# Kernel optimization log

Hardware: AMD Instinct MI355X
Metric: run time of the kernel (lower is better)

## Reference

```python
import jax, jax.numpy as jnp
import numpy as np

N, IN_F, OUT_F = 8192, 512, 256
NEG_INF = -9e15
LEAKY_SLOPE = 0.25


def setup_inputs() -> dict:
    key = jax.random.key(0)
    k1, k2, k3, k4, k5, k6 = jax.random.split(key, 6)
    inp = {
        "input": jax.random.normal(k1, (N, IN_F), dtype=jnp.float32),
        "adj": jax.random.randint(k2, (N, N), 0, 2, dtype=jnp.int32),
        # learned params (xavier-normal-ish scale)
        "weights": jax.random.normal(k3, (IN_F, OUT_F), dtype=jnp.float32) * (2.0 / (IN_F + OUT_F)) ** 0.5,
        "a1": jax.random.normal(k4, (OUT_F, 1), dtype=jnp.float32) * (2.0 / (OUT_F + 1)) ** 0.5,
        "a2": jax.random.normal(k5, (OUT_F, 1), dtype=jnp.float32) * (2.0 / (OUT_F + 1)) ** 0.5,
        "bias": jax.random.uniform(k6, (OUT_F,), dtype=jnp.float32, minval=-1.0 / OUT_F ** 0.5, maxval=1.0 / OUT_F ** 0.5),
    }
    return inp


def reference(input, adj, weights, a1, a2, bias):
    # h = input @ W  : [N, out]
    h = input @ weights
    # e[i,j] = leaky_relu((h@a1)[i] + (h@a2)[j])  : [N, N] via broadcast
    e1 = h @ a1  # [N,1]
    e2 = h @ a2  # [N,1]
    e = e1 + e2.T
    e = jnp.where(e > 0, e, LEAKY_SLOPE * e)
    # mask non-edges, row softmax (dropout omitted: deterministic reference)
    scores = jnp.where(adj > 0, e, NEG_INF)
    attention = jax.nn.softmax(scores, axis=1)
    # aggregate + bias
    return attention @ h + bias
```

## Files before the change

### kernel.cpp

```cpp
#include <hip/hip_runtime.h>
#include <hip/hip_fp16.h>

typedef __attribute__((ext_vector_type(8))) short short8;
typedef __attribute__((ext_vector_type(4))) float floatx4;
typedef __attribute__((ext_vector_type(4))) unsigned int uintx4;
typedef __attribute__((ext_vector_type(2))) unsigned int uintx2;
typedef __attribute__((ext_vector_type(4))) int intx4;
typedef __attribute__((ext_vector_type(4))) unsigned short ushortx4;
typedef unsigned int u32;

#define NN 8192
#define KIN 512
#define COUT 256
#define SHIFT 16.0f

#define AS1 __attribute__((address_space(1)))
#define AS3 __attribute__((address_space(3)))

__device__ __forceinline__ void stage16(const void* g, void* l) {
  __builtin_amdgcn_global_load_lds((const AS1 u32*)g, (AS3 u32*)l, 16, 0, 0);
}

__device__ __forceinline__ unsigned int f2bf(float f) {
  unsigned int u = __float_as_uint(f);
  return (u + 0x7FFFu + ((u >> 16) & 1u)) >> 16;
}

__device__ __forceinline__ u32 pkbf(float lo, float hi) {
  u32 a = __float_as_uint(lo) + 0x8000u;
  u32 b = __float_as_uint(hi) + 0x8000u;
  return __builtin_amdgcn_perm(b, a, 0x07060302u);
}

__device__ __forceinline__ short8 pack8(const float* p) {
  uintx4 w;
  w.x = pkbf(p[0], p[1]);
  w.y = pkbf(p[2], p[3]);
  w.z = pkbf(p[4], p[5]);
  w.w = pkbf(p[6], p[7]);
  union { uintx4 u; short8 s; } cv; cv.u = w;
  return cv.s;
}

__global__ void k_cast_input(const float* __restrict__ in, ushortx4* __restrict__ out) {
  int idx = blockIdx.x * 256 + threadIdx.x;
  floatx4 v = ((const floatx4*)in)[idx];
  ushortx4 o;
  o.x = (unsigned short)f2bf(v.x);
  o.y = (unsigned short)f2bf(v.y);
  o.z = (unsigned short)f2bf(v.z);
  o.w = (unsigned short)f2bf(v.w);
  out[idx] = o;
}

__global__ void k_prep_w(const float* __restrict__ w, unsigned short* __restrict__ wt) {
  int idx = blockIdx.x * 256 + threadIdx.x;
  int k = idx >> 8, c = idx & 255;
  wt[c * KIN + k] = (unsigned short)f2bf(w[idx]);
}

__global__ __launch_bounds__(256)
void k_gemm_h(const unsigned short* __restrict__ inA, const unsigned short* __restrict__ wt,
              const float* __restrict__ a1, const float* __restrict__ a2,
              unsigned short* __restrict__ ht, float* __restrict__ e1, float* __restrict__ e2,
              float* __restrict__ A1, float* __restrict__ A2, u32* __restrict__ e2pk) {
  int wave = threadIdx.x >> 6;
  int lane = threadIdx.x & 63;
  int n = lane & 15, q = lane >> 4;
  int row0 = blockIdx.x * 64 + wave * 16;
  int mrow = row0 + n;

  floatx4 acc[16];
#pragma unroll
  for (int t = 0; t < 16; ++t) acc[t] = (floatx4){0.f, 0.f, 0.f, 0.f};

  for (int kc = 0; kc < KIN / 32; ++kc) {
    int k0 = kc * 32 + q * 8;
    short8 a = *(const short8*)(inA + (size_t)mrow * KIN + k0);
#pragma unroll
    for (int nt = 0; nt < 16; ++nt) {
      short8 b = *(const short8*)(wt + (size_t)(nt * 16 + n) * KIN + k0);
      acc[nt] = __builtin_amdgcn_mfma_f32_16x16x32_bf16(a, b, acc[nt], 0, 0, 0);
    }
  }

  int i0 = row0 + q * 4;
#pragma unroll
  for (int nt = 0; nt < 16; ++nt) {
    int c = nt * 16 + n;
    uintx2 pk;
    pk.x = f2bf(acc[nt][0]) | (f2bf(acc[nt][1]) << 16);
    pk.y = f2bf(acc[nt][2]) | (f2bf(acc[nt][3]) << 16);
    *(uintx2*)(ht + (size_t)c * NN + i0) = pk;
  }

  float s1[4] = {0.f, 0.f, 0.f, 0.f}, s2[4] = {0.f, 0.f, 0.f, 0.f};
#pragma unroll
  for (int nt = 0; nt < 16; ++nt) {
    float w1 = a1[nt * 16 + n];
    float w2 = a2[nt * 16 + n];
#pragma unroll
    for (int r = 0; r < 4; ++r) {
      s1[r] += acc[nt][r] * w1;
      s2[r] += acc[nt][r] * w2;
    }
  }
#pragma unroll
  for (int m = 1; m < 16; m <<= 1) {
#pragma unroll
    for (int r = 0; r < 4; ++r) {
      s1[r] += __shfl_xor(s1[r], m);
      s2[r] += __shfl_xor(s2[r], m);
    }
  }
  if (n == 0) {
#pragma unroll
    for (int r = 0; r < 4; ++r) {
      float v1 = s1[r], v2 = s2[r];
      e1[i0 + r] = v1;
      e2[i0 + r] = v2;
      A1[i0 + r] = __expf(v1 - 8.0f);
      A2[i0 + r] = __expf(0.25f * v1 - 8.0f);
      u32 b1 = f2bf(__expf(v2 - 8.0f));
      u32 b2 = f2bf(__expf(0.25f * v2 - 8.0f));
      e2pk[i0 + r] = (b1 << 16) | b2;
    }
  }
}

__global__ __launch_bounds__(256, 2)
void k_attn_fused(const int* __restrict__ adj, const unsigned short* __restrict__ ht,
                  const float* __restrict__ A1, const float* __restrict__ A2,
                  const u32* __restrict__ e2pk,
                  __half2* __restrict__ oph, float* __restrict__ Dpart) {
  __shared__ __align__(16) char smem[69632];
  u32* e2s = (u32*)(smem + 65536);

  int b = blockIdx.x;
  int rg = b >> 3, js = b & 7;
  int wave = threadIdx.x >> 6, lane = threadIdx.x & 63;
  int n = lane & 15, q = lane >> 4;
  int rowblock = rg * 128;
  int rowbase = rowblock + wave * 32;
  int jbeg = js * 1024;

  ((uintx4*)e2s)[threadIdx.x] = *(const uintx4*)(e2pk + jbeg + threadIdx.x * 4);

  float A1v0 = A1[rowbase + n],      A2v0 = A2[rowbase + n];
  float A1v1 = A1[rowbase + 16 + n], A2v1 = A2[rowbase + 16 + n];

  floatx4 acc[2][16];
  floatx4 accd[2];
#pragma unroll
  for (int t = 0; t < 2; ++t) {
    accd[t] = (floatx4){0.f, 0.f, 0.f, 0.f};
#pragma unroll
    for (int nt = 0; nt < 16; ++nt) acc[t][nt] = (floatx4){0.f, 0.f, 0.f, 0.f};
  }

  union { uintx4 u; short8 s; } onesu;
  onesu.u = (uintx4){0x3F803F80u, 0x3F803F80u, 0x3F803F80u, 0x3F803F80u};
  short8 ones = onesu.s;

  auto stage = [&](int ch, int buf) {
    int j0g = jbeg + ch * 32;
    char* hbase = smem + buf * 32768;
#pragma unroll
    for (int i = 0; i < 4; ++i) {
      int seg = wave * 256 + i * 64 + lane;
      int c = seg >> 2;
      int j8 = (seg & 3) * 8;
      stage16(ht + (size_t)c * NN + j0g + j8, hbase + (size_t)(wave * 256 + i * 64) * 16);
    }
    char* abase = hbase + 16384 + wave * 4096;
    const int* aw = adj + (size_t)(rowblock + wave * 32) * NN + j0g;
#pragma unroll
    for (int i = 0; i < 4; ++i) {
      stage16(aw + (size_t)(i * 8 + (lane & 7)) * NN + (lane >> 3) * 4, abase + i * 1024);
    }
  };

  int rlo = n & 7, rhi = n >> 3;

  stage(0, 0);
  asm volatile("s_waitcnt lgkmcnt(0)" ::: "memory");
  asm volatile("s_barrier" ::: "memory");

  for (int ch = 0; ch < 32; ++ch) {
    int cur = ch & 1;
    if (ch < 31) {
      stage(ch + 1, cur ^ 1);
      asm volatile("s_waitcnt vmcnt(8)" ::: "memory");
    } else {
      asm volatile("s_waitcnt vmcnt(0)" ::: "memory");
    }

    const char* ab = smem + cur * 32768 + 16384 + wave * 4096;
    intx4 a0a = *(const intx4*)(ab + rhi * 1024 + q * 256 + rlo * 16);
    intx4 a0b = *(const intx4*)(ab + rhi * 1024 + q * 256 + 128 + rlo * 16);
    intx4 a1a = *(const intx4*)(ab + 2048 + rhi * 1024 + q * 256 + rlo * 16);
    intx4 a1b = *(const intx4*)(ab + 2048 + rhi * 1024 + q * 256 + 128 + rlo * 16);

    uintx4 ba = *(const uintx4*)(e2s + ch * 32 + q * 8);
    uintx4 bb = *(const uintx4*)(e2s + ch * 32 + q * 8 + 4);
    u32 bw[8] = {ba.x, ba.y, ba.z, ba.w, bb.x, bb.y, bb.z, bb.w};

    float p0[8], p1[8];
#pragma unroll
    for (int jj = 0; jj < 8; ++jj) {
      int av0 = (jj < 4) ? a0a[jj] : a0b[jj - 4];
      int av1 = (jj < 4) ? a1a[jj] : a1b[jj - 4];
      float B1 = __uint_as_float(bw[jj] & 0xffff0000u);
      float B2 = __uint_as_float(bw[jj] << 16);
      float m10 = A1v0 * B1, m20 = A2v0 * B2;
      float m11 = A1v1 * B1, m21 = A2v1 * B2;
      float pm0 = fmaxf(m10, m20);
      float pm1 = fmaxf(m11, m21);
      p0[jj] = (av0 != 0) ? pm0 : 0.f;
      p1[jj] = (av1 != 0) ? pm1 : 0.f;
    }
    short8 af0 = pack8(p0);
    short8 af1 = pack8(p1);

    asm volatile("s_barrier" ::: "memory");

    const short8* lb = (const short8*)(smem + (size_t)cur * 32768);
#pragma unroll
    for (int t = 0; t < 16; ++t) {
      short8 bf = lb[t * 64 + n * 4 + q];
      acc[0][t] = __builtin_amdgcn_mfma_f32_16x16x32_bf16(af0, bf, acc[0][t], 0, 0, 0);
      acc[1][t] = __builtin_amdgcn_mfma_f32_16x16x32_bf16(af1, bf, acc[1][t], 0, 0, 0);
    }
    accd[0] = __builtin_amdgcn_mfma_f32_16x16x32_bf16(af0, ones, accd[0], 0, 0, 0);
    accd[1] = __builtin_amdgcn_mfma_f32_16x16x32_bf16(af1, ones, accd[1], 0, 0, 0);

    asm volatile("s_waitcnt lgkmcnt(0)" ::: "memory");
    asm volatile("s_barrier" ::: "memory");
  }

  if (n == 0) {
#pragma unroll
    for (int t2 = 0; t2 < 2; ++t2)
#pragma unroll
      for (int r = 0; r < 4; ++r)
        Dpart[(size_t)js * NN + rowbase + t2 * 16 + q * 4 + r] = accd[t2][r];
  }

#pragma unroll
  for (int t2 = 0; t2 < 2; ++t2) {
    int ibase = rowbase + t2 * 16 + q * 4;
#pragma unroll
    for (int nt = 0; nt < 16; ++nt) {
      int c = nt * 16 + n;
      oph[((size_t)js * 4096 + (ibase >> 1)) * 256 + c] =
          __floats2half2_rn(acc[t2][nt][0], acc[t2][nt][1]);
      oph[((size_t)js * 4096 + (ibase >> 1) + 1) * 256 + c] =
          __floats2half2_rn(acc[t2][nt][2], acc[t2][nt][3]);
    }
  }
}

__global__ void k_final_part(float* __restrict__ out, const __half2* __restrict__ oph,
                             const float* __restrict__ Dpart, const float* __restrict__ bias) {
  int i = blockIdx.x;
  int c = threadIdx.x;
  int hi = i & 1;
  float s = 0.f, d = 0.f;
#pragma unroll
  for (int js = 0; js < 8; ++js) {
    __half2 h2 = oph[((size_t)js * 4096 + (i >> 1)) * 256 + c];
    s += hi ? __high2float(h2) : __low2float(h2);
    d += Dpart[(size_t)js * NN + i];
  }
  out[(size_t)i * COUT + c] = s / fmaxf(d, 1e-37f) + bias[c];
}

__global__ __launch_bounds__(256, 2)
void k_attn_atomic(const int* __restrict__ adj, const unsigned short* __restrict__ ht,
                   const float* __restrict__ e1, const float* __restrict__ e2,
                   float* __restrict__ out_num, float* __restrict__ Dbuf) {
  int b = blockIdx.x;
  int rg = b >> 3, js = b & 7;
  int wave = threadIdx.x >> 6, lane = threadIdx.x & 63;
  int n = lane & 15, q = lane >> 4;
  int rowbase = rg * 128 + wave * 32;

  float e1v0 = e1[rowbase + n];
  float e1v1 = e1[rowbase + 16 + n];

  floatx4 acc[2][16];
#pragma unroll
  for (int t = 0; t < 2; ++t)
#pragma unroll
    for (int nt = 0; nt < 16; ++nt) acc[t][nt] = (floatx4){0.f, 0.f, 0.f, 0.f};

  float d0 = 0.f, d1 = 0.f;
  int jbeg = js * 1024;

  for (int ch = 0; ch < 32; ++ch) {
    int j0 = jbeg + ch * 32 + q * 8;
    floatx4 ea = *(const floatx4*)(e2 + j0);
    floatx4 eb = *(const floatx4*)(e2 + j0 + 4);
    float ev[8] = {ea.x, ea.y, ea.z, ea.w, eb.x, eb.y, eb.z, eb.w};

    intx4 A00 = *(const intx4*)(adj + (size_t)(rowbase + n) * NN + j0);
    intx4 A01 = *(const intx4*)(adj + (size_t)(rowbase + n) * NN + j0 + 4);
    intx4 A10 = *(const intx4*)(adj + (size_t)(rowbase + 16 + n) * NN + j0);
    intx4 A11 = *(const intx4*)(adj + (size_t)(rowbase + 16 + n) * NN + j0 + 4);

    float p0[8], p1[8];
#pragma unroll
    for (int jj = 0; jj < 8; ++jj) {
      int av0 = (jj < 4) ? A00[jj] : A01[jj - 4];
      int av1 = (jj < 4) ? A10[jj] : A11[jj - 4];
      float t0 = e1v0 + ev[jj];
      float t1 = e1v1 + ev[jj];
      float f0 = fmaxf(t0, 0.25f * t0);
      float f1 = fmaxf(t1, 0.25f * t1);
      float x0 = __expf(f0 - SHIFT);
      float x1 = __expf(f1 - SHIFT);
      p0[jj] = (av0 != 0) ? x0 : 0.f;
      p1[jj] = (av1 != 0) ? x1 : 0.f;
      d0 += p0[jj];
      d1 += p1[jj];
    }
    short8 af0 = pack8(p0);
    short8 af1 = pack8(p1);

#pragma unroll
    for (int g = 0; g < 2; ++g) {
      short8 bf[8];
#pragma unroll
      for (int t = 0; t < 8; ++t)
        bf[t] = *(const short8*)(ht + (size_t)((g * 8 + t) * 16 + n) * NN + j0);
#pragma unroll
      for (int t = 0; t < 8; ++t) {
        acc[0][g * 8 + t] = __builtin_amdgcn_mfma_f32_16x16x32_bf16(af0, bf[t], acc[0][g * 8 + t], 0, 0, 0);
        acc[1][g * 8 + t] = __builtin_amdgcn_mfma_f32_16x16x32_bf16(af1, bf[t], acc[1][g * 8 + t], 0, 0, 0);
      }
    }
  }

  d0 += __shfl_xor(d0, 16); d0 += __shfl_xor(d0, 32);
  d1 += __shfl_xor(d1, 16); d1 += __shfl_xor(d1, 32);
  if (lane < 16) {
    atomicAdd(Dbuf + rowbase + lane, d0);
    atomicAdd(Dbuf + rowbase + 16 + lane, d1);
  }

#pragma unroll
  for (int t2 = 0; t2 < 2; ++t2) {
#pragma unroll
    for (int nt = 0; nt < 16; ++nt) {
#pragma unroll
      for (int r = 0; r < 4; ++r) {
        int i = rowbase + t2 * 16 + q * 4 + r;
        atomicAdd(out_num + (size_t)i * COUT + nt * 16 + n, acc[t2][nt][r]);
      }
    }
  }
}

__global__ void k_final_atomic(float* __restrict__ out, const float* __restrict__ Dbuf,
                               const float* __restrict__ bias) {
  int idx = blockIdx.x * 256 + threadIdx.x;
  int i = idx >> 8, c = idx & 255;
  float d = fmaxf(Dbuf[i], 1e-37f);
  out[idx] = out[idx] / d + bias[c];
}

extern "C" void kernel_launch(void* const* d_in, const int* in_sizes, int n_in,
                              void* d_out, int out_size, void* d_ws, size_t ws_size,
                              hipStream_t stream) {
  const float* input   = (const float*)d_in[0];
  const int*   adj     = (const int*)d_in[1];
  const float* weights = (const float*)d_in[2];
  const float* a1      = (const float*)d_in[3];
  const float* a2      = (const float*)d_in[4];
  const float* bias    = (const float*)d_in[5];
  float* out = (float*)d_out;
  char* ws = (char*)d_ws;

  unsigned short* inA = (unsigned short*)(ws);
  unsigned short* wt  = (unsigned short*)(ws + 8388608);
  unsigned short* ht  = (unsigned short*)(ws + 8650752);
  float* e1    = (float*)(ws + 12845056);
  float* e2    = (float*)(ws + 12877824);
  float* A1    = (float*)(ws + 12910592);
  float* A2    = (float*)(ws + 12943360);
  u32*   e2pk  = (u32*)  (ws + 12976128);
  float* Dpart = (float*)(ws + 13008896);
  __half2* oph = (__half2*)(ws + 13271040);
  const size_t WS_NEEDED_PART = 13271040 + (size_t)8 * NN * COUT * 2;
  float* Dbuf = Dpart;

  k_cast_input<<<4096, 256, 0, stream>>>(input, (ushortx4*)inA);
  k_prep_w<<<512, 256, 0, stream>>>(weights, wt);
  k_gemm_h<<<128, 256, 0, stream>>>(inA, wt, a1, a2, ht, e1, e2, A1, A2, e2pk);

  if (ws_size >= WS_NEEDED_PART) {
    k_attn_fused<<<512, 256, 0, stream>>>(adj, ht, A1, A2, e2pk, oph, Dpart);
    k_final_part<<<8192, 256, 0, stream>>>(out, oph, Dpart, bias);
  } else {
    hipMemsetAsync(out, 0, (size_t)NN * COUT * sizeof(float), stream);
    hipMemsetAsync(Dbuf, 0, NN * sizeof(float), stream);
    k_attn_atomic<<<512, 256, 0, stream>>>(adj, ht, e1, e2, out, Dbuf);
    k_final_atomic<<<8192, 256, 0, stream>>>(out, Dbuf, bias);
  }
}
```

Measured before the change: 447.3 us.

## Pre-pack adjacency into a bitmask and merge the prep kernels

A combined prep kernel now does the input and weight bf16 casts and also packs the int32 adjacency matrix into one bit per edge. The attention kernel then loads a small per-block bitmask into LDS once, instead of staging int32 adjacency tiles every chunk. This frees LDS, reduces per-chunk global loads to the h tiles only, and moves the wait so it overlaps the probability computation. The cost is an extra streaming pass over adj, an extra bitmask buffer, and a larger workspace requirement; if the workspace is too small, the atomic fallback path runs instead.

Measured after the change: 466.7 us. 1.04x slower.

```diff
diff --git a/kernel.cpp b/kernel.cpp
--- a/kernel.cpp
+++ b/kernel.cpp
@@ -42,21 +42,38 @@
   return cv.s;
 }
 
-__global__ void k_cast_input(const float* __restrict__ in, ushortx4* __restrict__ out) {
-  int idx = blockIdx.x * 256 + threadIdx.x;
-  floatx4 v = ((const floatx4*)in)[idx];
-  ushortx4 o;
-  o.x = (unsigned short)f2bf(v.x);
-  o.y = (unsigned short)f2bf(v.y);
-  o.z = (unsigned short)f2bf(v.z);
-  o.w = (unsigned short)f2bf(v.w);
-  out[idx] = o;
-}
-
-__global__ void k_prep_w(const float* __restrict__ w, unsigned short* __restrict__ wt) {
-  int idx = blockIdx.x * 256 + threadIdx.x;
-  int k = idx >> 8, c = idx & 255;
-  wt[c * KIN + k] = (unsigned short)f2bf(w[idx]);
+__global__ __launch_bounds__(256)
+void k_prep(const float* __restrict__ in, ushortx4* __restrict__ inA4,
+            const float* __restrict__ w, unsigned short* __restrict__ wt,
+            const int* __restrict__ adj, u32* __restrict__ abit, int do_pack) {
+  int b = blockIdx.x;
+  if (b < 4096) {
+    int idx = b * 256 + threadIdx.x;
+    floatx4 v = ((const floatx4*)in)[idx];
+    ushortx4 o;
+    o.x = (unsigned short)f2bf(v.x);
+    o.y = (unsigned short)f2bf(v.y);
+    o.z = (unsigned short)f2bf(v.z);
+    o.w = (unsigned short)f2bf(v.w);
+    inA4[idx] = o;
+  } else if (b < 4608) {
+    int idx = (b - 4096) * 256 + threadIdx.x;
+    int k = idx >> 8, c = idx & 255;
+    wt[c * KIN + k] = (unsigned short)f2bf(w[idx]);
+  } else if (do_pack) {
+    int g = (b - 4608) * 256 + threadIdx.x;
+    const intx4* src = (const intx4*)adj + (size_t)g * 8;
+    u32 m = 0;
+#pragma unroll
+    for (int k = 0; k < 8; ++k) {
+      intx4 v = src[k];
+      m |= (u32)(v.x != 0) << (k * 4);
+      m |= (u32)(v.y != 0) << (k * 4 + 1);
+      m |= (u32)(v.z != 0) << (k * 4 + 2);
+      m |= (u32)(v.w != 0) << (k * 4 + 3);
+    }
+    abit[g] = m;
+  }
 }
 
 __global__ __launch_bounds__(256)
@@ -129,12 +146,13 @@
 }
 
 __global__ __launch_bounds__(256, 2)
-void k_attn_fused(const int* __restrict__ adj, const unsigned short* __restrict__ ht,
+void k_attn_fused(const u32* __restrict__ abit, const unsigned short* __restrict__ ht,
                   const float* __restrict__ A1, const float* __restrict__ A2,
                   const u32* __restrict__ e2pk,
                   __half2* __restrict__ oph, float* __restrict__ Dpart) {
-  __shared__ __align__(16) char smem[69632];
-  u32* e2s = (u32*)(smem + 65536);
+  __shared__ __align__(16) char smem[55296];
+  u32* e2s  = (u32*)(smem + 32768);
+  u32* bits = (u32*)(smem + 36864);
 
   int b = blockIdx.x;
   int rg = b >> 3, js = b & 7;
@@ -144,27 +162,9 @@
   int rowbase = rowblock + wave * 32;
   int jbeg = js * 1024;
 
-  ((uintx4*)e2s)[threadIdx.x] = *(const uintx4*)(e2pk + jbeg + threadIdx.x * 4);
-
-  float A1v0 = A1[rowbase + n],      A2v0 = A2[rowbase + n];
-  float A1v1 = A1[rowbase + 16 + n], A2v1 = A2[rowbase + 16 + n];
-
-  floatx4 acc[2][16];
-  floatx4 accd[2];
-#pragma unroll
-  for (int t = 0; t < 2; ++t) {
-    accd[t] = (floatx4){0.f, 0.f, 0.f, 0.f};
-#pragma unroll
-    for (int nt = 0; nt < 16; ++nt) acc[t][nt] = (floatx4){0.f, 0.f, 0.f, 0.f};
-  }
-
-  union { uintx4 u; short8 s; } onesu;
-  onesu.u = (uintx4){0x3F803F80u, 0x3F803F80u, 0x3F803F80u, 0x3F803F80u};
-  short8 ones = onesu.s;
-
   auto stage = [&](int ch, int buf) {
     int j0g = jbeg + ch * 32;
-    char* hbase = smem + buf * 32768;
+    char* hbase = smem + buf * 16384;
 #pragma unroll
     for (int i = 0; i < 4; ++i) {
       int seg = wave * 256 + i * 64 + lane;
@@ -172,34 +172,48 @@
       int j8 = (seg & 3) * 8;
       stage16(ht + (size_t)c * NN + j0g + j8, hbase + (size_t)(wave * 256 + i * 64) * 16);
     }
-    char* abase = hbase + 16384 + wave * 4096;
-    const int* aw = adj + (size_t)(rowblock + wave * 32) * NN + j0g;
-#pragma unroll
-    for (int i = 0; i < 4; ++i) {
-      stage16(aw + (size_t)(i * 8 + (lane & 7)) * NN + (lane >> 3) * 4, abase + i * 1024);
-    }
   };
 
-  int rlo = n & 7, rhi = n >> 3;
-
   stage(0, 0);
+
+  ((uintx4*)e2s)[threadIdx.x] = *(const uintx4*)(e2pk + jbeg + threadIdx.x * 4);
+
+  {
+    int r = threadIdx.x >> 1, half = threadIdx.x & 1;
+    const uintx4* src = (const uintx4*)(abit + (size_t)(rowblock + r) * 256 + js * 32 + half * 16);
+    uintx4* dst = (uintx4*)(bits + r * 36 + half * 16);
+#pragma unroll
+    for (int k2 = 0; k2 < 4; ++k2) dst[k2] = src[k2];
+  }
+
+  float A1v0 = A1[rowbase + n],      A2v0 = A2[rowbase + n];
+  float A1v1 = A1[rowbase + 16 + n], A2v1 = A2[rowbase + 16 + n];
+
+  floatx4 acc[2][16];
+  floatx4 accd[2];
+#pragma unroll
+  for (int t = 0; t < 2; ++t) {
+    accd[t] = (floatx4){0.f, 0.f, 0.f, 0.f};
+#pragma unroll
+    for (int nt = 0; nt < 16; ++nt) acc[t][nt] = (floatx4){0.f, 0.f, 0.f, 0.f};
+  }
+
+  union { uintx4 u; short8 s; } onesu;
+  onesu.u = (uintx4){0x3F803F80u, 0x3F803F80u, 0x3F803F80u, 0x3F803F80u};
+  short8 ones = onesu.s;
+
   asm volatile("s_waitcnt lgkmcnt(0)" ::: "memory");
   asm volatile("s_barrier" ::: "memory");
 
+  int row0i = (wave * 32 + n) * 36;
+  int row1i = (wave * 32 + 16 + n) * 36;
+
   for (int ch = 0; ch < 32; ++ch) {
     int cur = ch & 1;
-    if (ch < 31) {
-      stage(ch + 1, cur ^ 1);
-      asm volatile("s_waitcnt vmcnt(8)" ::: "memory");
-    } else {
-      asm volatile("s_waitcnt vmcnt(0)" ::: "memory");
-    }
-
-    const char* ab = smem + cur * 32768 + 16384 + wave * 4096;
-    intx4 a0a = *(const intx4*)(ab + rhi * 1024 + q * 256 + rlo * 16);
-    intx4 a0b = *(const intx4*)(ab + rhi * 1024 + q * 256 + 128 + rlo * 16);
-    intx4 a1a = *(const intx4*)(ab + 2048 + rhi * 1024 + q * 256 + rlo * 16);
-    intx4 a1b = *(const intx4*)(ab + 2048 + rhi * 1024 + q * 256 + 128 + rlo * 16);
+    if (ch < 31) stage(ch + 1, cur ^ 1);
+
+    u32 f0 = (bits[row0i + ch] >> (q * 8)) & 0xffu;
+    u32 f1 = (bits[row1i + ch] >> (q * 8)) & 0xffu;
 
     uintx4 ba = *(const uintx4*)(e2s + ch * 32 + q * 8);
     uintx4 bb = *(const uintx4*)(e2s + ch * 32 + q * 8 + 4);
@@ -208,23 +222,26 @@
     float p0[8], p1[8];
 #pragma unroll
     for (int jj = 0; jj < 8; ++jj) {
-      int av0 = (jj < 4) ? a0a[jj] : a0b[jj - 4];
-      int av1 = (jj < 4) ? a1a[jj] : a1b[jj - 4];
       float B1 = __uint_as_float(bw[jj] & 0xffff0000u);
       float B2 = __uint_as_float(bw[jj] << 16);
       float m10 = A1v0 * B1, m20 = A2v0 * B2;
       float m11 = A1v1 * B1, m21 = A2v1 * B2;
       float pm0 = fmaxf(m10, m20);
       float pm1 = fmaxf(m11, m21);
-      p0[jj] = (av0 != 0) ? pm0 : 0.f;
-      p1[jj] = (av1 != 0) ? pm1 : 0.f;
+      p0[jj] = (f0 & (1u << jj)) ? pm0 : 0.f;
+      p1[jj] = (f1 & (1u << jj)) ? pm1 : 0.f;
     }
     short8 af0 = pack8(p0);
     short8 af1 = pack8(p1);
 
+    if (ch < 31) {
+      asm volatile("s_waitcnt vmcnt(4)" ::: "memory");
+    } else {
+      asm volatile("s_waitcnt vmcnt(0)" ::: "memory");
+    }
     asm volatile("s_barrier" ::: "memory");
 
-    const short8* lb = (const short8*)(smem + (size_t)cur * 32768);
+    const short8* lb = (const short8*)(smem + (size_t)cur * 16384);
 #pragma unroll
     for (int t = 0; t < 16; ++t) {
       short8 bf = lb[t * 64 + n * 4 + q];
@@ -391,17 +408,18 @@
   u32*   e2pk  = (u32*)  (ws + 12976128);
   float* Dpart = (float*)(ws + 13008896);
   __half2* oph = (__half2*)(ws + 13271040);
-  const size_t WS_NEEDED_PART = 13271040 + (size_t)8 * NN * COUT * 2;
+  u32*   abit  = (u32*)  (ws + 46825472);
+  const size_t WS_NEEDED_PART = 46825472 + (size_t)NN * (NN / 32) * 4;
   float* Dbuf = Dpart;
 
-  k_cast_input<<<4096, 256, 0, stream>>>(input, (ushortx4*)inA);
-  k_prep_w<<<512, 256, 0, stream>>>(weights, wt);
-  k_gemm_h<<<128, 256, 0, stream>>>(inA, wt, a1, a2, ht, e1, e2, A1, A2, e2pk);
-
   if (ws_size >= WS_NEEDED_PART) {
-    k_attn_fused<<<512, 256, 0, stream>>>(adj, ht, A1, A2, e2pk, oph, Dpart);
+    k_prep<<<12800, 256, 0, stream>>>(input, (ushortx4*)inA, weights, wt, adj, abit, 1);
+    k_gemm_h<<<128, 256, 0, stream>>>(inA, wt, a1, a2, ht, e1, e2, A1, A2, e2pk);
+    k_attn_fused<<<512, 256, 0, stream>>>(abit, ht, A1, A2, e2pk, oph, Dpart);
     k_final_part<<<8192, 256, 0, stream>>>(out, oph, Dpart, bias);
   } else {
+    k_prep<<<4608, 256, 0, stream>>>(input, (ushortx4*)inA, weights, wt, adj, abit, 0);
+    k_gemm_h<<<128, 256, 0, stream>>>(inA, wt, a1, a2, ht, e1, e2, A1, A2, e2pk);
     hipMemsetAsync(out, 0, (size_t)NN * COUT * sizeof(float), stream);
     hipMemsetAsync(Dbuf, 0, NN * sizeof(float), stream);
     k_attn_atomic<<<512, 256, 0, stream>>>(adj, ht, e1, e2, out, Dbuf);
```

## Load adjacency and h directly from global memory instead of LDS double-buffering

Applied to the files above, without the earlier changes.

The attention kernel drops its LDS double-buffered staging of adjacency tiles, h tiles and e2 values, and instead reads them with per-lane vector global loads straight into registers. This removes the barriers and LDS traffic, but loses the software prefetch overlap. The h operand is now re-read from global/L2 by every wave with strided 16-byte accesses, which risks exposing latency. The two preprocessing cast kernels are also merged into one launch.

Measured after the change: 508.4 us. 13.7% more time.

```diff
diff --git a/kernel.cpp b/kernel.cpp
--- a/kernel.cpp
+++ b/kernel.cpp
@@ -13,13 +13,6 @@
 #define KIN 512
 #define COUT 256
 #define SHIFT 16.0f
-
-#define AS1 __attribute__((address_space(1)))
-#define AS3 __attribute__((address_space(3)))
-
-__device__ __forceinline__ void stage16(const void* g, void* l) {
-  __builtin_amdgcn_global_load_lds((const AS1 u32*)g, (AS3 u32*)l, 16, 0, 0);
-}
 
 __device__ __forceinline__ unsigned int f2bf(float f) {
   unsigned int u = __float_as_uint(f);
@@ -42,21 +35,24 @@
   return cv.s;
 }
 
-__global__ void k_cast_input(const float* __restrict__ in, ushortx4* __restrict__ out) {
-  int idx = blockIdx.x * 256 + threadIdx.x;
-  floatx4 v = ((const floatx4*)in)[idx];
-  ushortx4 o;
-  o.x = (unsigned short)f2bf(v.x);
-  o.y = (unsigned short)f2bf(v.y);
-  o.z = (unsigned short)f2bf(v.z);
-  o.w = (unsigned short)f2bf(v.w);
-  out[idx] = o;
-}
-
-__global__ void k_prep_w(const float* __restrict__ w, unsigned short* __restrict__ wt) {
-  int idx = blockIdx.x * 256 + threadIdx.x;
-  int k = idx >> 8, c = idx & 255;
-  wt[c * KIN + k] = (unsigned short)f2bf(w[idx]);
+__global__ __launch_bounds__(256)
+void k_prep(const float* __restrict__ in, ushortx4* __restrict__ inA4,
+            const float* __restrict__ w, unsigned short* __restrict__ wt) {
+  int b = blockIdx.x;
+  if (b < 4096) {
+    int idx = b * 256 + threadIdx.x;
+    floatx4 v = ((const floatx4*)in)[idx];
+    ushortx4 o;
+    o.x = (unsigned short)f2bf(v.x);
+    o.y = (unsigned short)f2bf(v.y);
+    o.z = (unsigned short)f2bf(v.z);
+    o.w = (unsigned short)f2bf(v.w);
+    inA4[idx] = o;
+  } else {
+    int idx = (b - 4096) * 256 + threadIdx.x;
+    int k = idx >> 8, c = idx & 255;
+    wt[c * KIN + k] = (unsigned short)f2bf(w[idx]);
+  }
 }
 
 __global__ __launch_bounds__(256)
@@ -129,22 +125,16 @@
 }
 
 __global__ __launch_bounds__(256, 2)
-void k_attn_fused(const int* __restrict__ adj, const unsigned short* __restrict__ ht,
-                  const float* __restrict__ A1, const float* __restrict__ A2,
-                  const u32* __restrict__ e2pk,
-                  __half2* __restrict__ oph, float* __restrict__ Dpart) {
-  __shared__ __align__(16) char smem[69632];
-  u32* e2s = (u32*)(smem + 65536);
-
+void k_attn_direct(const int* __restrict__ adj, const unsigned short* __restrict__ ht,
+                   const float* __restrict__ A1, const float* __restrict__ A2,
+                   const u32* __restrict__ e2pk,
+                   __half2* __restrict__ oph, float* __restrict__ Dpart) {
   int b = blockIdx.x;
   int rg = b >> 3, js = b & 7;
   int wave = threadIdx.x >> 6, lane = threadIdx.x & 63;
   int n = lane & 15, q = lane >> 4;
-  int rowblock = rg * 128;
-  int rowbase = rowblock + wave * 32;
+  int rowbase = rg * 128 + wave * 32;
   int jbeg = js * 1024;
-
-  ((uintx4*)e2s)[threadIdx.x] = *(const uintx4*)(e2pk + jbeg + threadIdx.x * 4);
 
   float A1v0 = A1[rowbase + n],      A2v0 = A2[rowbase + n];
   float A1v1 = A1[rowbase + 16 + n], A2v1 = A2[rowbase + 16 + n];
@@ -162,54 +152,27 @@
   onesu.u = (uintx4){0x3F803F80u, 0x3F803F80u, 0x3F803F80u, 0x3F803F80u};
   short8 ones = onesu.s;
 
-  auto stage = [&](int ch, int buf) {
-    int j0g = jbeg + ch * 32;
-    char* hbase = smem + buf * 32768;
-#pragma unroll
-    for (int i = 0; i < 4; ++i) {
-      int seg = wave * 256 + i * 64 + lane;
-      int c = seg >> 2;
-      int j8 = (seg & 3) * 8;
-      stage16(ht + (size_t)c * NN + j0g + j8, hbase + (size_t)(wave * 256 + i * 64) * 16);
-    }
-    char* abase = hbase + 16384 + wave * 4096;
-    const int* aw = adj + (size_t)(rowblock + wave * 32) * NN + j0g;
-#pragma unroll
-    for (int i = 0; i < 4; ++i) {
-      stage16(aw + (size_t)(i * 8 + (lane & 7)) * NN + (lane >> 3) * 4, abase + i * 1024);
-    }
-  };
-
-  int rlo = n & 7, rhi = n >> 3;
-
-  stage(0, 0);
-  asm volatile("s_waitcnt lgkmcnt(0)" ::: "memory");
-  asm volatile("s_barrier" ::: "memory");
+  const int* ar0 = adj + (size_t)(rowbase + n) * NN + jbeg + q * 8;
+  const int* ar1 = adj + (size_t)(rowbase + 16 + n) * NN + jbeg + q * 8;
+  const u32* ep  = e2pk + jbeg + q * 8;
+  const unsigned short* hb = ht + (size_t)n * NN + jbeg + q * 8;
 
   for (int ch = 0; ch < 32; ++ch) {
-    int cur = ch & 1;
-    if (ch < 31) {
-      stage(ch + 1, cur ^ 1);
-      asm volatile("s_waitcnt vmcnt(8)" ::: "memory");
-    } else {
-      asm volatile("s_waitcnt vmcnt(0)" ::: "memory");
-    }
-
-    const char* ab = smem + cur * 32768 + 16384 + wave * 4096;
-    intx4 a0a = *(const intx4*)(ab + rhi * 1024 + q * 256 + rlo * 16);
-    intx4 a0b = *(const intx4*)(ab + rhi * 1024 + q * 256 + 128 + rlo * 16);
-    intx4 a1a = *(const intx4*)(ab + 2048 + rhi * 1024 + q * 256 + rlo * 16);
-    intx4 a1b = *(const intx4*)(ab + 2048 + rhi * 1024 + q * 256 + 128 + rlo * 16);
-
-    uintx4 ba = *(const uintx4*)(e2s + ch * 32 + q * 8);
-    uintx4 bb = *(const uintx4*)(e2s + ch * 32 + q * 8 + 4);
+    int jo = ch * 32;
+
+    intx4 A00 = *(const intx4*)(ar0 + jo);
+    intx4 A01 = *(const intx4*)(ar0 + jo + 4);
+    intx4 A10 = *(const intx4*)(ar1 + jo);
+    intx4 A11 = *(const intx4*)(ar1 + jo + 4);
+    uintx4 ba = *(const uintx4*)(ep + jo);
+    uintx4 bb = *(const uintx4*)(ep + jo + 4);
     u32 bw[8] = {ba.x, ba.y, ba.z, ba.w, bb.x, bb.y, bb.z, bb.w};
 
     float p0[8], p1[8];
 #pragma unroll
     for (int jj = 0; jj < 8; ++jj) {
-      int av0 = (jj < 4) ? a0a[jj] : a0b[jj - 4];
-      int av1 = (jj < 4) ? a1a[jj] : a1b[jj - 4];
+      int av0 = (jj < 4) ? A00[jj] : A01[jj - 4];
+      int av1 = (jj < 4) ? A10[jj] : A11[jj - 4];
       float B1 = __uint_as_float(bw[jj] & 0xffff0000u);
       float B2 = __uint_as_float(bw[jj] << 16);
       float m10 = A1v0 * B1, m20 = A2v0 * B2;
@@ -222,20 +185,14 @@
     short8 af0 = pack8(p0);
     short8 af1 = pack8(p1);
 
-    asm volatile("s_barrier" ::: "memory");
-
-    const short8* lb = (const short8*)(smem + (size_t)cur * 32768);
 #pragma unroll
     for (int t = 0; t < 16; ++t) {
-      short8 bf = lb[t * 64 + n * 4 + q];
-      acc[0][t] = __builtin_amdgcn_mfma_f32_16x16x32_bf16(af0, bf, acc[0][t], 0, 0, 0);
-      acc[1][t] = __builtin_amdgcn_mfma_f32_16x16x32_bf16(af1, bf, acc[1][t], 0, 0, 0);
+      short8 bfv = *(const short8*)(hb + (size_t)(t * 16) * NN + jo);
+      acc[0][t] = __builtin_amdgcn_mfma_f32_16x16x32_bf16(af0, bfv, acc[0][t], 0, 0, 0);
+      acc[1][t] = __builtin_amdgcn_mfma_f32_16x16x32_bf16(af1, bfv, acc[1][t], 0, 0, 0);
     }
     accd[0] = __builtin_amdgcn_mfma_f32_16x16x32_bf16(af0, ones, accd[0], 0, 0, 0);
     accd[1] = __builtin_amdgcn_mfma_f32_16x16x32_bf16(af1, ones, accd[1], 0, 0, 0);
-
-    asm volatile("s_waitcnt lgkmcnt(0)" ::: "memory");
-    asm volatile("s_barrier" ::: "memory");
   }
 
   if (n == 0) {
@@ -394,12 +351,11 @@
   const size_t WS_NEEDED_PART = 13271040 + (size_t)8 * NN * COUT * 2;
   float* Dbuf = Dpart;
 
-  k_cast_input<<<4096, 256, 0, stream>>>(input, (ushortx4*)inA);
-  k_prep_w<<<512, 256, 0, stream>>>(weights, wt);
+  k_prep<<<4608, 256, 0, stream>>>(input, (ushortx4*)inA, weights, wt);
   k_gemm_h<<<128, 256, 0, stream>>>(inA, wt, a1, a2, ht, e1, e2, A1, A2, e2pk);
 
   if (ws_size >= WS_NEEDED_PART) {
-    k_attn_fused<<<512, 256, 0, stream>>>(adj, ht, A1, A2, e2pk, oph, Dpart);
+    k_attn_direct<<<512, 256, 0, stream>>>(adj, ht, A1, A2, e2pk, oph, Dpart);
     k_final_part<<<8192, 256, 0, stream>>>(out, oph, Dpart, bias);
   } else {
     hipMemsetAsync(out, 0, (size_t)NN * COUT * sizeof(float), stream);
```
